# Performance work log

Hardware: AMD Instinct MI355X
Metric: run time of the kernel (lower is better)

## Reference

```python
import jax, jax.numpy as jnp
import numpy as np

VOCAB_SIZES = [100000] * 26
EMBED_DIM = 128
BOT_DIMS = [512, 256, 128]
TOP_DIMS = [1024, 1024, 512, 256, 1]
N_DENSE = 13
BATCH = 8192


def setup_inputs() -> dict:
    key = jax.random.key(0)
    ks = jax.random.split(key, 32)
    inp = {}
    inp['dense_features'] = jax.random.normal(ks[0], (BATCH, N_DENSE), dtype=jnp.float32)
    inp['cat_features'] = jax.random.randint(ks[1], (BATCH, 26), 0, VOCAB_SIZES[0], dtype=jnp.int32)
    total_vocab = sum(VOCAB_SIZES)
    inp['embedding_table'] = jax.random.uniform(ks[2], (total_vocab, EMBED_DIM), dtype=jnp.float32,
                                               minval=-1.0, maxval=1.0) * (3.0 / EMBED_DIM) ** 0.5
    # Bottom MLP params
    fan_in = N_DENSE
    for i, d in enumerate(BOT_DIMS):
        inp[f'W{i}'] = jax.random.normal(ks[3 + i], (fan_in, d), dtype=jnp.float32) * (2.0 / (fan_in + d)) ** 0.5
        inp[f'b{i}'] = jax.random.normal(ks[8 + i], (d,), dtype=jnp.float32) * (1.0 / d) ** 0.5
        fan_in = d
    # Top MLP params; input dim = 128 + 27*28/2 = 506
    n_feat = 1 + len(VOCAB_SIZES)
    fan_in = BOT_DIMS[-1] + n_feat * (n_feat + 1) // 2
    for i, d in enumerate(TOP_DIMS):
        inp[f'T{i}'] = jax.random.normal(ks[14 + i], (fan_in, d), dtype=jnp.float32) * (2.0 / (fan_in + d)) ** 0.5
        inp[f'tb{i}'] = jax.random.normal(ks[22 + i], (d,), dtype=jnp.float32) * (1.0 / d) ** 0.5
        fan_in = d
    return inp


def reference(dense_features, cat_features, embedding_table,
              W0, b0, W1, b1, W2, b2,
              T0, tb0, T1, tb1, T2, tb2, T3, tb3, T4, tb4):
    B = dense_features.shape[0]
    # Bottom MLP
    x = dense_features
    for W, b in ((W0, b0), (W1, b1), (W2, b2)):
        x = jax.nn.relu(x @ W + b)
    bot_out = x  # [B, 128]
    feature_stack = bot_out.reshape(B, -1, EMBED_DIM)  # [B, 1, 128]
    # Embedding lookup with per-table offsets into concatenated table
    offsets = jnp.asarray(np.concatenate([[0], np.cumsum(VOCAB_SIZES[:-1])]), dtype=jnp.int32)
    idx = (cat_features + offsets[None, :]).reshape(-1)
    embed = embedding_table[idx].reshape(B, len(VOCAB_SIZES), EMBED_DIM)  # [B, 26, 128]
    feats = jnp.concatenate([feature_stack, embed], axis=1)  # [B, 27, 128]
    # Dot interaction: upper-triangular (incl. diag) entries of feats @ feats^T
    xactions = jnp.einsum('bnd,bmd->bnm', feats, feats)  # [B, 27, 27]
    iu, ju = jnp.triu_indices(feats.shape[1])
    dot_out = xactions[:, iu, ju]  # [B, 378] row-major upper-tri, same order as boolean-mask extraction
    top_in = jnp.concatenate([bot_out, dot_out], axis=-1)  # [B, 506]
    # Top MLP: relu on all but last layer, sigmoid on last
    tops = ((T0, tb0), (T1, tb1), (T2, tb2), (T3, tb3), (T4, tb4))
    x = top_in
    for i, (W, b) in enumerate(tops):
        x = x @ W + b
        x = jax.nn.sigmoid(x) if i == len(tops) - 1 else jax.nn.relu(x)
    return x
```

## Files before the change

### kernel.cpp

```cpp
#include <hip/hip_runtime.h>
#include <hip/hip_bf16.h>
#include <math.h>

#define BATCH 8192

typedef __bf16 bf16x8 __attribute__((ext_vector_type(8)));
typedef float f32x4 __attribute__((ext_vector_type(4)));

__device__ __forceinline__ unsigned short f2bf(float f) {
    unsigned int u = __float_as_uint(f);
    u = u + 0x7FFFu + ((u >> 16) & 1u);
    return (unsigned short)(u >> 16);
}
__device__ __forceinline__ float bf2f(unsigned short h) {
    return __uint_as_float(((unsigned int)h) << 16);
}
__device__ __forceinline__ void async16(const void* g, void* l) {
    __builtin_amdgcn_global_load_lds(
        (const __attribute__((address_space(1))) unsigned int*)g,
        (__attribute__((address_space(3))) unsigned int*)l, 16, 0, 0);
}

__global__ __launch_bounds__(256) void bottom13_kernel(
    const float* __restrict__ dense,
    const float* __restrict__ W0, const float* __restrict__ b0,
    unsigned short* __restrict__ h1)
{
    __shared__ float xs[8][16];
    const int t = threadIdx.x;
    const int row0 = blockIdx.x * 8;

    if (t < 8 * 13) {
        int r = t / 13, k = t % 13;
        xs[r][k] = dense[(size_t)(row0 + r) * 13 + k];
    }
    __syncthreads();

    #pragma unroll
    for (int jj = 0; jj < 2; ++jj) {
        const int j = t + jj * 256;
        float acc[8];
        const float bj = b0[j];
        #pragma unroll
        for (int r = 0; r < 8; ++r) acc[r] = bj;
        #pragma unroll
        for (int k = 0; k < 13; ++k) {
            float w = W0[k * 512 + j];
            #pragma unroll
            for (int r = 0; r < 8; ++r) acc[r] += xs[r][k] * w;
        }
        #pragma unroll
        for (int r = 0; r < 8; ++r)
            h1[(size_t)(row0 + r) * 512 + j] = f2bf(fmaxf(acc[r], 0.f));
    }
}

struct TransDesc { const float* W; unsigned short* Wt; int K, N, nkb, tile0; };
struct TransDescs { TransDesc d[6]; };

__global__ __launch_bounds__(256) void trans_all_kernel(TransDescs td)
{
    __shared__ float tile[32][33];
    const int b = blockIdx.x;
    int i = 0;
    #pragma unroll
    for (int q = 1; q < 6; ++q) if (b >= td.d[q].tile0) i = q;
    const TransDesc D = td.d[i];
    const int tl = b - D.tile0;
    const int kb = (tl % D.nkb) * 32;
    const int nb = (tl / D.nkb) * 32;
    const int Kpad = D.nkb * 32;
    const int tx = threadIdx.x & 31, ty = threadIdx.x >> 5;

    #pragma unroll
    for (int r = 0; r < 32; r += 8) {
        int k = kb + ty + r;
        tile[ty + r][tx] = (k < D.K) ? D.W[(size_t)k * D.N + nb + tx] : 0.f;
    }
    __syncthreads();
    #pragma unroll
    for (int r = 0; r < 32; r += 8) {
        D.Wt[(size_t)(nb + ty + r) * Kpad + kb + tx] = f2bf(tile[tx][ty + r]);
    }
}

__global__ __launch_bounds__(256) void interact_kernel(
    const int* __restrict__ cat,
    const float* __restrict__ table,
    const float* __restrict__ botf,
    unsigned short* __restrict__ A0)
{
    __shared__ float fs[27][132];
    __shared__ int idx[26];

    const int t = threadIdx.x;
    const int row = blockIdx.x;

    if (t < 26) idx[t] = cat[(size_t)row * 26 + t] + t * 100000;
    __syncthreads();

    for (int q = t; q < 27 * 32; q += 256) {
        const int i  = q >> 5;
        const int c4 = q & 31;
        const float* src = (i == 0) ? (botf + (size_t)row * 128)
                                    : (table + (size_t)idx[i - 1] * 128);
        float4 v = reinterpret_cast<const float4*>(src)[c4];
        fs[i][c4 * 4 + 0] = v.x;
        fs[i][c4 * 4 + 1] = v.y;
        fs[i][c4 * 4 + 2] = v.z;
        fs[i][c4 * 4 + 3] = v.w;
    }
    __syncthreads();

    for (int p = t; p < 378; p += 256) {
        int i = 0, rem = p;
        while (rem >= 27 - i) { rem -= 27 - i; ++i; }
        const int j = i + rem;
        float s = 0.f;
        for (int k = 0; k < 128; k += 4) {
            float4 a = *reinterpret_cast<const float4*>(&fs[i][k]);
            float4 b = *reinterpret_cast<const float4*>(&fs[j][k]);
            s += a.x * b.x + a.y * b.y + a.z * b.z + a.w * b.w;
        }
        A0[(size_t)row * 512 + 128 + p] = f2bf(s);
    }
    if (t < 6) A0[(size_t)row * 512 + 506 + t] = 0;
}

__global__ __launch_bounds__(256) void gemm_bf16_kernel(
    const unsigned short* __restrict__ A,
    const unsigned short* __restrict__ Bt,
    const float* __restrict__ bias,
    unsigned short* __restrict__ C,
    float* __restrict__ Cf,
    int K, int N, int ldc, int relu)
{
    __shared__ unsigned short As[128 * 64];
    __shared__ unsigned short Bs[128 * 64];

    const int t = threadIdx.x;
    const int lane = t & 63;
    const int wid = t >> 6;
    const int wr = wid >> 1, wc = wid & 1;
    const int row0 = blockIdx.x * 128;
    const int col0 = blockIdx.y * 128;

    const char* gA[4]; const char* gB[4];
    char* lA[4]; char* lB[4];
    #pragma unroll
    for (int q = 0; q < 4; ++q) {
        int l16 = q * 256 + t;
        int row = l16 >> 3, chunk = l16 & 7;
        int swz = chunk ^ (row & 7);
        gA[q] = (const char*)A  + ((size_t)(row0 + row) * K + swz * 8) * 2;
        gB[q] = (const char*)Bt + ((size_t)(col0 + row) * K + swz * 8) * 2;
        lA[q] = (char*)As + l16 * 16;
        lB[q] = (char*)Bs + l16 * 16;
    }

    const int kb = lane >> 4;
    const int r15 = lane & 15;
    int aoff[4][2], boff[4][2];
    #pragma unroll
    for (int m = 0; m < 4; ++m) {
        int r = wr * 64 + m * 16 + r15;
        int c = wc * 64 + m * 16 + r15;
        #pragma unroll
        for (int ks = 0; ks < 2; ++ks) {
            aoff[m][ks] = r * 128 + (((ks * 4 + kb) ^ (r & 7)) << 4);
            boff[m][ks] = c * 128 + (((ks * 4 + kb) ^ (c & 7)) << 4);
        }
    }

    f32x4 acc[4][4] = {};

    for (int k0 = 0; k0 < K; k0 += 64) {
        #pragma unroll
        for (int q = 0; q < 4; ++q) {
            async16(gA[q] + (size_t)k0 * 2, lA[q]);
            async16(gB[q] + (size_t)k0 * 2, lB[q]);
        }
        __syncthreads();

        #pragma unroll
        for (int ks = 0; ks < 2; ++ks) {
            bf16x8 af[4], bfr[4];
            #pragma unroll
            for (int m = 0; m < 4; ++m)
                af[m] = *reinterpret_cast<const bf16x8*>((const char*)As + aoff[m][ks]);
            #pragma unroll
            for (int n = 0; n < 4; ++n)
                bfr[n] = *reinterpret_cast<const bf16x8*>((const char*)Bs + boff[n][ks]);

            #pragma unroll
            for (int m = 0; m < 4; ++m)
                #pragma unroll
                for (int n = 0; n < 4; ++n)
                    acc[m][n] = __builtin_amdgcn_mfma_f32_16x16x32_bf16(
                        af[m], bfr[n], acc[m][n], 0, 0, 0);
        }
        __syncthreads();
    }

    #pragma unroll
    for (int n = 0; n < 4; ++n) {
        const int col_g = col0 + wc * 64 + n * 16 + r15;
        const float bn = bias[col_g];
        #pragma unroll
        for (int m = 0; m < 4; ++m) {
            const int row_base = row0 + wr * 64 + m * 16 + (lane >> 4) * 4;
            #pragma unroll
            for (int reg = 0; reg < 4; ++reg) {
                float v = acc[m][n][reg] + bn;
                if (relu) v = fmaxf(v, 0.f);
                C[(size_t)(row_base + reg) * ldc + col_g] = f2bf(v);
                if (Cf) Cf[(size_t)(row_base + reg) * N + col_g] = v;
            }
        }
    }
}

__global__ __launch_bounds__(256) void final_layer_kernel(
    const unsigned short* __restrict__ A,
    const float* __restrict__ T4,
    const float* __restrict__ tb4,
    float* __restrict__ out)
{
    const int t = threadIdx.x;
    const int lane = t & 63;
    const int wave = t >> 6;
    const int row = blockIdx.x * 4 + wave;

    ushort4 a4 = reinterpret_cast<const ushort4*>(A + (size_t)row * 256)[lane];
    float4 w = reinterpret_cast<const float4*>(T4)[lane];
    float s = bf2f(a4.x) * w.x + bf2f(a4.y) * w.y + bf2f(a4.z) * w.z + bf2f(a4.w) * w.w;
    #pragma unroll
    for (int off = 32; off > 0; off >>= 1) s += __shfl_down(s, off, 64);
    if (lane == 0) out[row] = 1.f / (1.f + expf(-(s + tb4[0])));
}

extern "C" void kernel_launch(void* const* d_in, const int* in_sizes, int n_in,
                              void* d_out, int out_size, void* d_ws, size_t ws_size,
                              hipStream_t stream)
{
    const float* dense = (const float*)d_in[0];
    const int*   cat   = (const int*)d_in[1];
    const float* table = (const float*)d_in[2];
    const float* W0 = (const float*)d_in[3];
    const float* b0 = (const float*)d_in[4];
    const float* W1 = (const float*)d_in[5];
    const float* b1 = (const float*)d_in[6];
    const float* W2 = (const float*)d_in[7];
    const float* b2 = (const float*)d_in[8];
    const float* T0 = (const float*)d_in[9];
    const float* tb0 = (const float*)d_in[10];
    const float* T1 = (const float*)d_in[11];
    const float* tb1 = (const float*)d_in[12];
    const float* T2 = (const float*)d_in[13];
    const float* tb2 = (const float*)d_in[14];
    const float* T3 = (const float*)d_in[15];
    const float* tb3 = (const float*)d_in[16];
    const float* T4 = (const float*)d_in[17];
    const float* tb4 = (const float*)d_in[18];
    float* out = (float*)d_out;

    char* ws = (char*)d_ws;
    unsigned short* A0   = (unsigned short*)(ws);
    unsigned short* act1 = (unsigned short*)(ws + (((size_t)8)  << 20));
    unsigned short* act2 = (unsigned short*)(ws + (((size_t)24) << 20));
    float*          botf = (float*)(ws + (((size_t)40) << 20));
    unsigned short* h1   = (unsigned short*)(ws + (((size_t)44) << 20));
    unsigned short* h2   = (unsigned short*)(ws + (((size_t)52) << 20));
    unsigned short* W1t  = (unsigned short*)(ws + (((size_t)56) << 20));
    unsigned short* W2t  = (unsigned short*)(ws + (((size_t)57) << 20));
    unsigned short* T0t  = (unsigned short*)(ws + (((size_t)58) << 20));
    unsigned short* T1t  = (unsigned short*)(ws + (((size_t)60) << 20));
    unsigned short* T2t  = (unsigned short*)(ws + (((size_t)63) << 20));
    unsigned short* T3t  = (unsigned short*)(ws + (((size_t)66) << 20));

    TransDescs td;
    td.d[0] = { W1, W1t,  512,  256, 16,    0 };
    td.d[1] = { W2, W2t,  256,  128,  8,  128 };
    td.d[2] = { T0, T0t,  506, 1024, 16,  160 };
    td.d[3] = { T1, T1t, 1024, 1024, 32,  672 };
    td.d[4] = { T2, T2t, 1024,  512, 32, 1696 };
    td.d[5] = { T3, T3t,  512,  256, 16, 2208 };
    const int total_tiles = 2336;
    hipLaunchKernelGGL(trans_all_kernel, dim3(total_tiles), dim3(256), 0, stream, td);

    hipLaunchKernelGGL(bottom13_kernel, dim3(BATCH / 8), dim3(256), 0, stream,
                       dense, W0, b0, h1);

    hipLaunchKernelGGL(gemm_bf16_kernel, dim3(BATCH / 128, 256 / 128), dim3(256), 0, stream,
                       h1, W1t, b1, h2, (float*)nullptr, 512, 256, 256, 1);

    hipLaunchKernelGGL(gemm_bf16_kernel, dim3(BATCH / 128, 1), dim3(256), 0, stream,
                       h2, W2t, b2, A0, botf, 256, 128, 512, 1);

    hipLaunchKernelGGL(interact_kernel, dim3(BATCH), dim3(256), 0, stream,
                       cat, table, botf, A0);

    hipLaunchKernelGGL(gemm_bf16_kernel, dim3(BATCH / 128, 1024 / 128), dim3(256), 0, stream,
                       A0, T0t, tb0, act1, (float*)nullptr, 512, 1024, 1024, 1);
    hipLaunchKernelGGL(gemm_bf16_kernel, dim3(BATCH / 128, 1024 / 128), dim3(256), 0, stream,
                       act1, T1t, tb1, act2, (float*)nullptr, 1024, 1024, 1024, 1);
    hipLaunchKernelGGL(gemm_bf16_kernel, dim3(BATCH / 128, 512 / 128), dim3(256), 0, stream,
                       act2, T2t, tb2, act1, (float*)nullptr, 1024, 512, 512, 1);
    hipLaunchKernelGGL(gemm_bf16_kernel, dim3(BATCH / 128, 256 / 128), dim3(256), 0, stream,
                       act1, T3t, tb3, act2, (float*)nullptr, 512, 256, 256, 1);

    hipLaunchKernelGGL(final_layer_kernel, dim3(BATCH / 4), dim3(256), 0, stream,
                       act2, T4, tb4, out);
}
```

Before: 153.7 us.

## Double-buffer LDS tiles in bf16 GEMM to overlap global loads with MFMA

```diff
diff --git a/kernel.cpp b/kernel.cpp
--- a/kernel.cpp
+++ b/kernel.cpp
@@ -135,8 +135,8 @@
     float* __restrict__ Cf,
     int K, int N, int ldc, int relu)
 {
-    __shared__ unsigned short As[128 * 64];
-    __shared__ unsigned short Bs[128 * 64];
+    __shared__ unsigned short As[2][128 * 64];
+    __shared__ unsigned short Bs[2][128 * 64];
 
     const int t = threadIdx.x;
     const int lane = t & 63;
@@ -146,7 +146,7 @@
     const int col0 = blockIdx.y * 128;
 
     const char* gA[4]; const char* gB[4];
-    char* lA[4]; char* lB[4];
+    int ldst[4];
     #pragma unroll
     for (int q = 0; q < 4; ++q) {
         int l16 = q * 256 + t;
@@ -154,8 +154,7 @@
         int swz = chunk ^ (row & 7);
         gA[q] = (const char*)A  + ((size_t)(row0 + row) * K + swz * 8) * 2;
         gB[q] = (const char*)Bt + ((size_t)(col0 + row) * K + swz * 8) * 2;
-        lA[q] = (char*)As + l16 * 16;
-        lB[q] = (char*)Bs + l16 * 16;
+        ldst[q] = l16 * 16;
     }
 
     const int kb = lane >> 4;
@@ -174,23 +173,37 @@
 
     f32x4 acc[4][4] = {};
 
-    for (int k0 = 0; k0 < K; k0 += 64) {
-        #pragma unroll
-        for (int q = 0; q < 4; ++q) {
-            async16(gA[q] + (size_t)k0 * 2, lA[q]);
-            async16(gB[q] + (size_t)k0 * 2, lB[q]);
-        }
-        __syncthreads();
-
+    const int nt = K >> 6;
+
+    #pragma unroll
+    for (int q = 0; q < 4; ++q) {
+        async16(gA[q], (char*)As[0] + ldst[q]);
+        async16(gB[q], (char*)Bs[0] + ldst[q]);
+    }
+    __syncthreads();
+
+    int cur = 0;
+    for (int tt = 0; tt < nt; ++tt) {
+        if (tt + 1 < nt) {
+            const size_t koff = (size_t)(tt + 1) * 64 * 2;
+            #pragma unroll
+            for (int q = 0; q < 4; ++q) {
+                async16(gA[q] + koff, (char*)As[cur ^ 1] + ldst[q]);
+                async16(gB[q] + koff, (char*)Bs[cur ^ 1] + ldst[q]);
+            }
+        }
+
+        const char* aB = (const char*)As[cur];
+        const char* bB = (const char*)Bs[cur];
         #pragma unroll
         for (int ks = 0; ks < 2; ++ks) {
             bf16x8 af[4], bfr[4];
             #pragma unroll
             for (int m = 0; m < 4; ++m)
-                af[m] = *reinterpret_cast<const bf16x8*>((const char*)As + aoff[m][ks]);
+                af[m] = *reinterpret_cast<const bf16x8*>(aB + aoff[m][ks]);
             #pragma unroll
             for (int n = 0; n < 4; ++n)
-                bfr[n] = *reinterpret_cast<const bf16x8*>((const char*)Bs + boff[n][ks]);
+                bfr[n] = *reinterpret_cast<const bf16x8*>(bB + boff[n][ks]);
 
             #pragma unroll
             for (int m = 0; m < 4; ++m)
@@ -200,6 +213,7 @@
                         af[m], bfr[n], acc[m][n], 0, 0, 0);
         }
         __syncthreads();
+        cur ^= 1;
     }
 
     #pragma unroll
```

New measurement: 149.2 us. 1.03x faster.
